# Performance work log

Hardware: AMD Instinct MI355X
Metric: run time of the kernel (lower is better)

Reference implementation:

```python
import jax, jax.numpy as jnp
import numpy as np

D_MODEL = 512
D_FF = 2048
NUM_EXPERTS = 8
TOP_K = 2


def setup_inputs() -> dict:
    key = jax.random.key(0)
    k_x, k_r, k_w1, k_w2 = jax.random.split(key, 4)
    x = jax.random.normal(k_x, (4, 2048, D_MODEL), dtype=jnp.float32)
    # router: Linear(d_model -> num_experts, bias=False); weight [E, D]
    Wr = jax.random.normal(k_r, (NUM_EXPERTS, D_MODEL), dtype=jnp.float32) * (1.0 / np.sqrt(D_MODEL))
    # expert weights: W1 [E, d_ff, d_model], W2 [E, d_model, d_ff] (torch Linear layout)
    W1 = jax.random.normal(k_w1, (NUM_EXPERTS, D_FF, D_MODEL), dtype=jnp.float32) * (1.0 / np.sqrt(D_MODEL))
    W2 = jax.random.normal(k_w2, (NUM_EXPERTS, D_MODEL, D_FF), dtype=jnp.float32) * (1.0 / np.sqrt(D_FF))
    return {"x": x, "Wr": Wr, "W1": W1, "W2": W2}


def reference(x, Wr, W1, W2):
    B, L, D = x.shape
    T = B * L
    x_flat = x.reshape(T, D)

    # Router: logits -> softmax -> top-k -> scatter back to dense [T, E]
    logits = x_flat @ Wr.T  # router_temperature = 1.0
    sm = jax.nn.softmax(logits, axis=-1)
    top_v, top_i = jax.lax.top_k(sm, TOP_K)  # [T, k]
    probs = jnp.zeros_like(sm).at[jnp.arange(T)[:, None], top_i].set(top_v)

    # All-expert FFN (dense, as in the original): h = GELU(x W1^T), y = h W2^T
    h = jnp.einsum('td,efd->tef', x_flat, W1)  # [T, E, d_ff]
    h = jax.nn.gelu(h, approximate=False)      # torch nn.GELU default = exact erf
    expert_out = jnp.einsum('tef,edf->ted', h, W2)  # [T, E, D]

    # Weighted combine over experts (dropout is identity in eval mode)
    out = jnp.einsum('te,ted->td', probs, expert_out)
    return out.reshape(B, L, D)
```

## Files before the change

kernel.cpp:

```cpp
#include <hip/hip_runtime.h>
#include <hip/hip_bf16.h>
#include <math.h>

#define D_MODEL 512
#define D_FF    2048
#define NE      8
#define T_TOK   8192

typedef __attribute__((ext_vector_type(8))) short bf16x8;
typedef __attribute__((ext_vector_type(4))) float f32x4;

static __device__ __forceinline__ unsigned short f2bf(float f){
    union { float f; unsigned u; } v; v.f = f;
    unsigned r = v.u + 0x7FFFu + ((v.u >> 16) & 1u);
    return (unsigned short)(r >> 16);
}
static __device__ __forceinline__ float bf2f(unsigned short u){
    union { unsigned u; float f; } v; v.u = ((unsigned)u) << 16; return v.f;
}

static __device__ __forceinline__ float gelu_f(float x){
    float z = 0.7978845608028654f * (x + 0.044715f * x * x * x);
    float e = __builtin_amdgcn_exp2f(z * 2.8853900817779268f);
    float t = 1.f - 2.f * __builtin_amdgcn_rcpf(e + 1.f);
    return 0.5f * x * (1.f + t);
}

static __device__ __forceinline__ void gload16(const void* g, void* l){
    __builtin_amdgcn_global_load_lds((const __attribute__((address_space(1))) unsigned int*)g,
                                     (__attribute__((address_space(3))) unsigned int*)l, 16, 0, 0);
}

__global__ __launch_bounds__(256) void cvt2_f32_bf16(const float* __restrict__ s1,
                                                     unsigned short* __restrict__ d1,
                                                     const float* __restrict__ s2,
                                                     unsigned short* __restrict__ d2,
                                                     int n4){
    int i = blockIdx.x * blockDim.x + threadIdx.x;
    int stride = gridDim.x * blockDim.x;
    for (; i < 2 * n4; i += stride){
        const float* s = (i < n4) ? s1 : s2;
        unsigned short* d = (i < n4) ? d1 : d2;
        int j = (i < n4) ? i : i - n4;
        float4 v = ((const float4*)s)[j];
        ushort4 o;
        o.x = f2bf(v.x); o.y = f2bf(v.y); o.z = f2bf(v.z); o.w = f2bf(v.w);
        ((ushort4*)d)[j] = o;
    }
}

__global__ __launch_bounds__(512) void router_kernel(const float* __restrict__ x,
                                                     const float* __restrict__ Wr,
                                                     unsigned short* __restrict__ x_bf,
                                                     float* __restrict__ pair_prob,
                                                     int* __restrict__ lists,
                                                     int* __restrict__ cnt){
    __shared__ int s_ei[128];

    int tid  = threadIdx.x;
    int wv   = tid >> 6;
    int lane = tid & 63;
    int tblk = blockIdx.x * 64;

    #pragma unroll 1
    for (int i = 0; i < 8; ++i){
        int tl = wv * 8 + i;
        int t  = tblk + tl;
        const float* xr = x + (size_t)t * D_MODEL;
        float xv[8];
        #pragma unroll
        for (int c = 0; c < 8; ++c) xv[c] = xr[lane + 64*c];
        unsigned short* xb = x_bf + (size_t)t * D_MODEL;
        #pragma unroll
        for (int c = 0; c < 8; ++c) xb[lane + 64*c] = f2bf(xv[c]);
        float lg[NE];
        #pragma unroll
        for (int e = 0; e < NE; ++e){
            const float* wr = Wr + (size_t)e * D_MODEL;
            float s = 0.f;
            #pragma unroll
            for (int c = 0; c < 8; ++c) s = fmaf(xv[c], wr[lane + 64*c], s);
            #pragma unroll
            for (int off = 32; off; off >>= 1) s += __shfl_xor(s, off);
            lg[e] = s;
        }
        if (lane == 0){
            float m = lg[0];
            #pragma unroll
            for (int e = 1; e < NE; ++e) m = fmaxf(m, lg[e]);
            float sum = 0.f;
            #pragma unroll
            for (int e = 0; e < NE; ++e) sum += expf(lg[e] - m);
            int i0 = 0; float v0 = lg[0];
            #pragma unroll
            for (int e = 1; e < NE; ++e) if (lg[e] > v0){ v0 = lg[e]; i0 = e; }
            int i1 = -1; float v1 = -1e30f;
            #pragma unroll
            for (int e = 0; e < NE; ++e) if (e != i0 && lg[e] > v1){ v1 = lg[e]; i1 = e; }
            float inv = 1.f / sum;
            pair_prob[2*t]   = expf(v0 - m) * inv;
            pair_prob[2*t+1] = expf(v1 - m) * inv;
            s_ei[2*tl]     = i0;
            s_ei[2*tl + 1] = i1;
        }
    }
    __syncthreads();

    if (wv == 0){
        int e0 = s_ei[lane];
        int e1 = s_ei[64 + lane];
        unsigned long long below = (lane == 63) ? ~0ull >> 1 : (1ull << lane) - 1;
        unsigned long long m0[NE];
        int rank0 = 0, rank1 = 0, tot = 0;
        #pragma unroll
        for (int ex = 0; ex < NE; ++ex){
            m0[ex] = __ballot(e0 == ex);
            if (e0 == ex) rank0 = __popcll(m0[ex] & below);
        }
        #pragma unroll
        for (int ex = 0; ex < NE; ++ex){
            unsigned long long m1 = __ballot(e1 == ex);
            if (e1 == ex) rank1 = __popcll(m1 & below) + __popcll(m0[ex]);
            if (lane == ex) tot = __popcll(m0[ex]) + __popcll(m1);
        }
        int base_held = 0;
        if (lane < NE) base_held = atomicAdd(&cnt[lane], tot);
        int b0 = __shfl(base_held, e0);
        int b1 = __shfl(base_held, e1);
        int pairbase = blockIdx.x * 128;
        lists[e0 * T_TOK + b0 + rank0] = pairbase + lane;
        lists[e1 * T_TOK + b1 + rank1] = pairbase + 64 + lane;
    }
}


__global__ __launch_bounds__(256, 4) void gemm1_kernel(const unsigned short* __restrict__ x_bf,
                                                       const unsigned short* __restrict__ W1bf,
                                                       const float* __restrict__ pair_prob,
                                                       const int* __restrict__ lists,
                                                       const int* __restrict__ cnt,
                                                       unsigned short* __restrict__ H){
    __shared__ __align__(16) unsigned char lds_a[16384];
    __shared__ __align__(16) unsigned char lds_b[16384];
    __shared__ int   s_tok[128];
    __shared__ int   s_pair[128];
    __shared__ float s_prob[128];

    int bid = blockIdx.x;
    int q = bid >> 7, r = bid & 127;
    int tg = q * 8 + (r & 7);
    int f0 = (r >> 3) << 7;
    int e = -1, tm = 0, rem = tg;
    for (int i = 0; i < NE; ++i){
        int mt = (cnt[i] + 127) >> 7;
        if (e < 0){ if (rem < mt){ e = i; tm = rem; } else rem -= mt; }
    }
    if (e < 0) return;
    int ne = cnt[e];

    int tid = threadIdx.x;
    if (tid < 128){
        int idx = tm * 128 + tid;
        int pair = (idx < ne) ? lists[e * T_TOK + idx] : 0;
        s_pair[tid] = pair;
        s_tok[tid]  = (idx < ne) ? (pair >> 1) : 0;
        s_prob[tid] = (idx < ne) ? pair_prob[pair] : 0.f;
    }
    __syncthreads();

    int wv = tid >> 6, lane = tid & 63, l15 = lane & 15, lk = lane >> 4;
    int wm = wv >> 1, wn = wv & 1;

    int scol = (((lane & 7) ^ (lane >> 3)) << 3);
    const unsigned short* pa[4];
    const unsigned short* pb[4];
    #pragma unroll
    for (int j = 0; j < 4; ++j){
        int row = j * 32 + wv * 8 + (lane >> 3);
        pa[j] = x_bf + (size_t)s_tok[row] * D_MODEL + scol;
        pb[j] = W1bf + ((size_t)e * D_FF + f0 + row) * D_MODEL + scol;
    }
    int dstoff = wv * 1024;

    f32x4 zero4 = {0.f, 0.f, 0.f, 0.f};
    f32x4 acc[4][4];
    #pragma unroll
    for (int i = 0; i < 4; ++i)
        #pragma unroll
        for (int j = 0; j < 4; ++j) acc[i][j] = zero4;

    #pragma unroll 1
    for (int k = 0; k < 8; ++k){
        #pragma unroll
        for (int j = 0; j < 4; ++j){
            gload16(pa[j] + k * 64, lds_a + dstoff + j * 4096);
            gload16(pb[j] + k * 64, lds_b + dstoff + j * 4096);
        }
        asm volatile("s_waitcnt vmcnt(0)\n\ts_barrier" ::: "memory");
        #pragma unroll
        for (int kk = 0; kk < 2; ++kk){
            int co = (kk * 64 + lk * 16) ^ ((l15 & 7) << 4);
            bf16x8 a[4], b[4];
            #pragma unroll
            for (int mf = 0; mf < 4; ++mf)
                a[mf] = *(const bf16x8*)(lds_a + (wm * 64 + mf * 16 + l15) * 128 + co);
            #pragma unroll
            for (int nf = 0; nf < 4; ++nf)
                b[nf] = *(const bf16x8*)(lds_b + (wn * 64 + nf * 16 + l15) * 128 + co);
            #pragma unroll
            for (int mf = 0; mf < 4; ++mf)
                #pragma unroll
                for (int nf = 0; nf < 4; ++nf)
                    acc[mf][nf] = __builtin_amdgcn_mfma_f32_16x16x32_bf16(a[mf], b[nf], acc[mf][nf], 0, 0, 0);
        }
        asm volatile("s_waitcnt lgkmcnt(0)\n\ts_barrier" ::: "memory");
    }

    #pragma unroll
    for (int mf = 0; mf < 4; ++mf){
        #pragma unroll
        for (int rr = 0; rr < 4; ++rr){
            int trow = wm * 64 + mf * 16 + lk * 4 + rr;
            int idx  = tm * 128 + trow;
            if (idx < ne){
                float p = s_prob[trow];
                unsigned short* hrow = H + (size_t)s_pair[trow] * D_FF + f0 + wn * 64 + l15;
                #pragma unroll
                for (int nf = 0; nf < 4; ++nf)
                    hrow[nf * 16] = f2bf(p * gelu_f(acc[mf][nf][rr]));
            }
        }
    }
}

__global__ __launch_bounds__(256, 4) void gemm2_kernel(const unsigned short* __restrict__ H,
                                                       const unsigned short* __restrict__ W2bf,
                                                       const int* __restrict__ lists,
                                                       const int* __restrict__ cnt,
                                                       unsigned short* __restrict__ ybuf){
    __shared__ __align__(16) unsigned char lds_a[16384];
    __shared__ __align__(16) unsigned char lds_b[16384];
    __shared__ int s_pair[128];

    int bid = blockIdx.x;
    int q = bid >> 5, r = bid & 31;
    int tg = q * 8 + (r & 7);
    int d0 = (r >> 3) << 7;
    int e = -1, tm = 0, rem = tg;
    for (int i = 0; i < NE; ++i){
        int mt = (cnt[i] + 127) >> 7;
        if (e < 0){ if (rem < mt){ e = i; tm = rem; } else rem -= mt; }
    }
    if (e < 0) return;
    int ne = cnt[e];

    int tid = threadIdx.x;
    if (tid < 128){
        int idx = tm * 128 + tid;
        s_pair[tid] = (idx < ne) ? lists[e * T_TOK + idx] : 0;
    }
    __syncthreads();

    int wv = tid >> 6, lane = tid & 63, l15 = lane & 15, lk = lane >> 4;
    int wm = wv >> 1, wn = wv & 1;

    int scol = (((lane & 7) ^ (lane >> 3)) << 3);
    const unsigned short* pa[4];
    const unsigned short* pb[4];
    #pragma unroll
    for (int j = 0; j < 4; ++j){
        int row = j * 32 + wv * 8 + (lane >> 3);
        pa[j] = H + (size_t)s_pair[row] * D_FF + scol;
        pb[j] = W2bf + ((size_t)e * D_MODEL + d0 + row) * D_FF + scol;
    }
    int dstoff = wv * 1024;

    f32x4 zero4 = {0.f, 0.f, 0.f, 0.f};
    f32x4 acc[4][4];
    #pragma unroll
    for (int i = 0; i < 4; ++i)
        #pragma unroll
        for (int j = 0; j < 4; ++j) acc[i][j] = zero4;

    #pragma unroll 1
    for (int k = 0; k < 32; ++k){
        #pragma unroll
        for (int j = 0; j < 4; ++j){
            gload16(pa[j] + k * 64, lds_a + dstoff + j * 4096);
            gload16(pb[j] + k * 64, lds_b + dstoff + j * 4096);
        }
        asm volatile("s_waitcnt vmcnt(0)\n\ts_barrier" ::: "memory");
        #pragma unroll
        for (int kk = 0; kk < 2; ++kk){
            int co = (kk * 64 + lk * 16) ^ ((l15 & 7) << 4);
            bf16x8 a[4], b[4];
            #pragma unroll
            for (int mf = 0; mf < 4; ++mf)
                a[mf] = *(const bf16x8*)(lds_a + (wm * 64 + mf * 16 + l15) * 128 + co);
            #pragma unroll
            for (int nf = 0; nf < 4; ++nf)
                b[nf] = *(const bf16x8*)(lds_b + (wn * 64 + nf * 16 + l15) * 128 + co);
            #pragma unroll
            for (int mf = 0; mf < 4; ++mf)
                #pragma unroll
                for (int nf = 0; nf < 4; ++nf)
                    acc[mf][nf] = __builtin_amdgcn_mfma_f32_16x16x32_bf16(a[mf], b[nf], acc[mf][nf], 0, 0, 0);
        }
        asm volatile("s_waitcnt lgkmcnt(0)\n\ts_barrier" ::: "memory");
    }

    #pragma unroll
    for (int mf = 0; mf < 4; ++mf){
        #pragma unroll
        for (int rr = 0; rr < 4; ++rr){
            int trow = wm * 64 + mf * 16 + lk * 4 + rr;
            int idx  = tm * 128 + trow;
            if (idx < ne){
                unsigned short* yrow = ybuf + (size_t)s_pair[trow] * D_MODEL + d0 + wn * 64 + l15;
                #pragma unroll
                for (int nf = 0; nf < 4; ++nf)
                    yrow[nf * 16] = f2bf(acc[mf][nf][rr]);
            }
        }
    }
}

__global__ __launch_bounds__(256) void combine_kernel(const unsigned short* __restrict__ ybuf,
                                                      float* __restrict__ out){
    int gid  = blockIdx.x * 256 + threadIdx.x;
    int t    = gid >> 6;
    int lane = gid & 63;
    if (t >= T_TOK) return;
    const unsigned short* y0 = ybuf + (size_t)(2 * t) * D_MODEL + lane * 8;
    const unsigned short* y1 = y0 + D_MODEL;
    unsigned short a[8], b[8];
    *(int4*)a = *(const int4*)y0;
    *(int4*)b = *(const int4*)y1;
    float res[8];
    #pragma unroll
    for (int j = 0; j < 8; ++j) res[j] = bf2f(a[j]) + bf2f(b[j]);
    float* orow = out + (size_t)t * D_MODEL + lane * 8;
    *(float4*)(orow)     = *(float4*)(res);
    *(float4*)(orow + 4) = *(float4*)(res + 4);
}

__global__ __launch_bounds__(512, 2) void moe_ffn_fallback(const unsigned short* __restrict__ x_bf,
                                                           const unsigned short* __restrict__ W1bf,
                                                           const unsigned short* __restrict__ W2bf,
                                                           const float* __restrict__ pair_prob,
                                                           const int* __restrict__ lists,
                                                           const int* __restrict__ cnt,
                                                           float* __restrict__ out){
    __shared__ __align__(16) unsigned char lds_x[64 * 1024];
    __shared__ __align__(16) unsigned char lds_h[64 * 256];
    int bid  = blockIdx.x;
    int xcd  = bid & 7, slot = bid >> 3;
    int eA   = xcd >> 1, sA = xcd & 1;
    int eB   = eA + 4;
    int tA   = (cnt[eA] + 63) >> 6;
    int tB   = (cnt[eB] + 63) >> 6;
    int e, sp, tile;
    if (slot < tA)           { e = eA; sp = sA; tile = slot; }
    else if (slot < tA + tB) { e = eB; sp = sA; tile = slot - tA; }
    else return;
    int ne = cnt[e];
    int tid = threadIdx.x;
    {
        int row = tid >> 3;
        int idx = tile * 64 + row;
        int tok = 0;
        if (idx < ne) tok = lists[e * T_TOK + idx] >> 1;
        int seg = (tid & 7) * 64;
        const unsigned short* src = x_bf + (size_t)tok * D_MODEL + seg;
        int sw = (row & 7) << 4;
        #pragma unroll
        for (int g = 0; g < 8; ++g){
            int4 v = *(const int4*)(src + g * 8);
            int col2 = (seg + g * 8) * 2;
            *(int4*)(lds_x + row * 1024 + (col2 ^ sw)) = v;
        }
    }
    __syncthreads();
    int wv = tid >> 6, lane = tid & 63, l15 = lane & 15, lk = lane >> 4;
    int swz = (l15 & 7) << 4;
    f32x4 zero4 = {0.f, 0.f, 0.f, 0.f};
    f32x4 yacc[4][4];
    #pragma unroll
    for (int i = 0; i < 4; ++i)
        #pragma unroll
        for (int j = 0; j < 4; ++j) yacc[i][j] = zero4;
    const unsigned short* w1p0 = W1bf + ((size_t)e * D_FF + sp * 1024 + wv * 16 + l15) * D_MODEL + lk * 8;
    const unsigned short* w2p0 = W2bf + ((size_t)e * D_MODEL + wv * 64 + l15) * D_FF + sp * 1024 + lk * 8;
    for (int fc = 0; fc < 8; ++fc){
        f32x4 hacc[4];
        #pragma unroll
        for (int at = 0; at < 4; ++at) hacc[at] = zero4;
        const unsigned short* w1p = w1p0 + (size_t)(fc * 128) * D_MODEL;
        #pragma unroll
        for (int ks = 0; ks < 16; ++ks){
            bf16x8 bb = *(const bf16x8*)(w1p + ks * 32);
            int col2 = (ks * 32 + lk * 8) * 2;
            #pragma unroll
            for (int at = 0; at < 4; ++at){
                bf16x8 a = *(const bf16x8*)(lds_x + (at * 16 + l15) * 1024 + (col2 ^ swz));
                hacc[at] = __builtin_amdgcn_mfma_f32_16x16x32_bf16(a, bb, hacc[at], 0, 0, 0);
            }
        }
        {
            int fl2 = (wv * 16 + l15) * 2;
            #pragma unroll
            for (int at = 0; at < 4; ++at){
                #pragma unroll
                for (int rr = 0; rr < 4; ++rr){
                    int tok = at * 16 + lk * 4 + rr;
                    *(unsigned short*)(lds_h + tok * 256 + (fl2 ^ ((tok & 7) << 4))) = f2bf(gelu_f(hacc[at][rr]));
                }
            }
        }
        asm volatile("s_waitcnt lgkmcnt(0)\n\ts_barrier" ::: "memory");
        const unsigned short* w2p = w2p0 + fc * 128;
        #pragma unroll
        for (int ks2 = 0; ks2 < 4; ++ks2){
            int col2 = (ks2 * 32 + lk * 8) * 2;
            bf16x8 am[4];
            #pragma unroll
            for (int mt = 0; mt < 4; ++mt)
                am[mt] = *(const bf16x8*)(lds_h + (mt * 16 + l15) * 256 + (col2 ^ swz));
            #pragma unroll
            for (int nt = 0; nt < 4; ++nt){
                bf16x8 bb = *(const bf16x8*)(w2p + (size_t)nt * 16 * D_FF + ks2 * 32);
                #pragma unroll
                for (int mt = 0; mt < 4; ++mt)
                    yacc[mt][nt] = __builtin_amdgcn_mfma_f32_16x16x32_bf16(am[mt], bb, yacc[mt][nt], 0, 0, 0);
            }
        }
        asm volatile("s_waitcnt lgkmcnt(0)\n\ts_barrier" ::: "memory");
    }
    const int* lrow = lists + e * T_TOK + tile * 64;
    #pragma unroll
    for (int mt = 0; mt < 4; ++mt){
        #pragma unroll
        for (int rr = 0; rr < 4; ++rr){
            int trow = mt * 16 + lk * 4 + rr;
            int idx  = tile * 64 + trow;
            if (idx < ne){
                int pair = lrow[trow];
                float p  = pair_prob[pair];
                float* orow = out + (size_t)(pair >> 1) * D_MODEL;
                #pragma unroll
                for (int nt = 0; nt < 4; ++nt)
                    atomicAdd(orow + wv * 64 + nt * 16 + l15, p * yacc[mt][nt][rr]);
            }
        }
    }
}

extern "C" void kernel_launch(void* const* d_in, const int* in_sizes, int n_in,
                              void* d_out, int out_size, void* d_ws, size_t ws_size,
                              hipStream_t stream){
    const float* x  = (const float*)d_in[0];
    const float* Wr = (const float*)d_in[1];
    const float* W1 = (const float*)d_in[2];
    const float* W2 = (const float*)d_in[3];
    float* out = (float*)d_out;

    char* ws = (char*)d_ws;
    unsigned short* x_bf = (unsigned short*)(ws);
    unsigned short* W1bf = (unsigned short*)(ws + 8388608);
    unsigned short* W2bf = (unsigned short*)(ws + 25165824);
    unsigned short* H    = (unsigned short*)(ws + 41943040);
    float* pair_prob     = (float*)(ws + 109051904);
    int*   lists         = (int*)(ws + 109117440);
    int*   cnt           = (int*)(ws + 109379584);
    unsigned short* ybuf = (unsigned short*)(ws);
    const size_t NEED = 109379616;
    bool big = ws_size >= NEED;
    if (!big){
        pair_prob = (float*)(ws + 41943040);
        lists     = (int*)(ws + 42008576);
        cnt       = (int*)(ws + 42270720);
    }

    hipMemsetAsync(cnt, 0, NE * sizeof(int), stream);

    cvt2_f32_bf16<<<2048, 256, 0, stream>>>(W1, W1bf, W2, W2bf, (NE * D_FF * D_MODEL) / 4);

    router_kernel<<<T_TOK / 64, 512, 0, stream>>>(x, Wr, x_bf, pair_prob, lists, cnt);

    if (big){
        gemm1_kernel<<<17 * 128, 256, 0, stream>>>(x_bf, W1bf, pair_prob, lists, cnt, H);
        gemm2_kernel<<<17 * 32, 256, 0, stream>>>(H, W2bf, lists, cnt, ybuf);
        combine_kernel<<<(T_TOK * 64) / 256, 256, 0, stream>>>(ybuf, out);
    } else {
        hipMemsetAsync(d_out, 0, (size_t)out_size * sizeof(float), stream);
        moe_ffn_fallback<<<2080, 512, 0, stream>>>(x_bf, W1bf, W2bf, pair_prob, lists, cnt, out);
    }
}
```

Baseline: 147.3 us.

## Store H in expert-sorted, K-slab-major layout for contiguous GEMM2 loads

GEMM1 now writes the intermediate H at rows indexed by the expert-sorted position (prefix of expert counts plus tile row), split into 64-column K slabs, instead of scattering rows by pair id. GEMM2 then reads its A operand as contiguous rows per slab rather than gathering through the pair list. This is meant to turn gathered, row-strided H reads into dense, coalesced accesses with better cache locality. It relies on the pair index being recovered elsewhere during the final combine and on SLABU (16384 rows) covering all pairs.

```diff
diff --git a/kernel.cpp b/kernel.cpp
--- a/kernel.cpp
+++ b/kernel.cpp
@@ -6,6 +6,7 @@
 #define D_FF    2048
 #define NE      8
 #define T_TOK   8192
+#define SLABU   (16384 * 64)
 
 typedef __attribute__((ext_vector_type(8))) short bf16x8;
 typedef __attribute__((ext_vector_type(4))) float f32x4;
@@ -143,17 +144,17 @@
     __shared__ __align__(16) unsigned char lds_a[16384];
     __shared__ __align__(16) unsigned char lds_b[16384];
     __shared__ int   s_tok[128];
-    __shared__ int   s_pair[128];
     __shared__ float s_prob[128];
 
     int bid = blockIdx.x;
     int q = bid >> 7, r = bid & 127;
     int tg = q * 8 + (r & 7);
     int f0 = (r >> 3) << 7;
-    int e = -1, tm = 0, rem = tg;
+    int e = -1, tm = 0, rem = tg, pfx = 0;
     for (int i = 0; i < NE; ++i){
-        int mt = (cnt[i] + 127) >> 7;
-        if (e < 0){ if (rem < mt){ e = i; tm = rem; } else rem -= mt; }
+        int c = cnt[i];
+        int mt = (c + 127) >> 7;
+        if (e < 0){ if (rem < mt){ e = i; tm = rem; } else { rem -= mt; pfx += c; } }
     }
     if (e < 0) return;
     int ne = cnt[e];
@@ -162,7 +163,6 @@
     if (tid < 128){
         int idx = tm * 128 + tid;
         int pair = (idx < ne) ? lists[e * T_TOK + idx] : 0;
-        s_pair[tid] = pair;
         s_tok[tid]  = (idx < ne) ? (pair >> 1) : 0;
         s_prob[tid] = (idx < ne) ? pair_prob[pair] : 0.f;
     }
@@ -216,18 +216,21 @@
         asm volatile("s_waitcnt lgkmcnt(0)\n\ts_barrier" ::: "memory");
     }
 
-    #pragma unroll
-    for (int mf = 0; mf < 4; ++mf){
-        #pragma unroll
-        for (int rr = 0; rr < 4; ++rr){
-            int trow = wm * 64 + mf * 16 + lk * 4 + rr;
-            int idx  = tm * 128 + trow;
-            if (idx < ne){
-                float p = s_prob[trow];
-                unsigned short* hrow = H + (size_t)s_pair[trow] * D_FF + f0 + wn * 64 + l15;
-                #pragma unroll
-                for (int nf = 0; nf < 4; ++nf)
-                    hrow[nf * 16] = f2bf(p * gelu_f(acc[mf][nf][rr]));
+    {
+        unsigned short* hs = H + (size_t)((f0 >> 6) + wn) * SLABU + l15;
+        int gbase = pfx + tm * 128;
+        #pragma unroll
+        for (int mf = 0; mf < 4; ++mf){
+            #pragma unroll
+            for (int rr = 0; rr < 4; ++rr){
+                int trow = wm * 64 + mf * 16 + lk * 4 + rr;
+                if (tm * 128 + trow < ne){
+                    float p = s_prob[trow];
+                    unsigned short* hrow = hs + (size_t)(gbase + trow) * 64;
+                    #pragma unroll
+                    for (int nf = 0; nf < 4; ++nf)
+                        hrow[nf * 16] = f2bf(p * gelu_f(acc[mf][nf][rr]));
+                }
             }
         }
     }
@@ -246,10 +249,11 @@
     int q = bid >> 5, r = bid & 31;
     int tg = q * 8 + (r & 7);
     int d0 = (r >> 3) << 7;
-    int e = -1, tm = 0, rem = tg;
+    int e = -1, tm = 0, rem = tg, pfx = 0;
     for (int i = 0; i < NE; ++i){
-        int mt = (cnt[i] + 127) >> 7;
-        if (e < 0){ if (rem < mt){ e = i; tm = rem; } else rem -= mt; }
+        int c = cnt[i];
+        int mt = (c + 127) >> 7;
+        if (e < 0){ if (rem < mt){ e = i; tm = rem; } else { rem -= mt; pfx += c; } }
     }
     if (e < 0) return;
     int ne = cnt[e];
@@ -267,10 +271,11 @@
     int scol = (((lane & 7) ^ (lane >> 3)) << 3);
     const unsigned short* pa[4];
     const unsigned short* pb[4];
+    int gbase = pfx + tm * 128;
     #pragma unroll
     for (int j = 0; j < 4; ++j){
         int row = j * 32 + wv * 8 + (lane >> 3);
-        pa[j] = H + (size_t)s_pair[row] * D_FF + scol;
+        pa[j] = H + (size_t)(gbase + row) * 64 + scol;
         pb[j] = W2bf + ((size_t)e * D_MODEL + d0 + row) * D_FF + scol;
     }
     int dstoff = wv * 1024;
@@ -286,8 +291,8 @@
     for (int k = 0; k < 32; ++k){
         #pragma unroll
         for (int j = 0; j < 4; ++j){
-            gload16(pa[j] + k * 64, lds_a + dstoff + j * 4096);
-            gload16(pb[j] + k * 64, lds_b + dstoff + j * 4096);
+            gload16(pa[j] + (size_t)k * SLABU, lds_a + dstoff + j * 4096);
+            gload16(pb[j] + k * 64,            lds_b + dstoff + j * 4096);
         }
         asm volatile("s_waitcnt vmcnt(0)\n\ts_barrier" ::: "memory");
         #pragma unroll
```

Result: faster. 143.1 us (-2.8%).
